# Performance work log

Hardware: AMD Instinct MI355X
Metric: run time of the kernel (lower is better)

The kernel has to match this reference:

```python
import jax, jax.numpy as jnp
import numpy as np

N = 100000
E = 3200000
D_IN = 128
D_H = 128
K = 3


def setup_inputs() -> dict:
    key = jax.random.key(0)
    ks = jax.random.split(key, 8)
    x = jax.random.normal(ks[0], (N, D_IN), dtype=jnp.float32)
    src = jax.random.randint(ks[1], (E,), 0, N, dtype=jnp.int32)
    dst = jax.random.randint(ks[2], (E,), 0, N, dtype=jnp.int32)
    s = 1.0 / np.sqrt(D_H)
    W1 = jax.random.normal(ks[3], (D_IN, D_H), dtype=jnp.float32) * s
    b1 = jnp.zeros((D_H,), jnp.float32)
    W2 = jax.random.normal(ks[4], (D_H, D_H), dtype=jnp.float32) * s
    b2 = jnp.zeros((D_H,), jnp.float32)
    Wf1 = jax.random.normal(ks[5], (D_H, D_H), dtype=jnp.float32) * s
    bf1 = jnp.zeros((D_H,), jnp.float32)
    Wf2 = jax.random.normal(ks[6], (D_H, 1), dtype=jnp.float32) * s
    bf2 = jnp.zeros((1,), jnp.float32)
    return {"x": x, "src": src, "dst": dst, "W1": W1, "b1": b1, "W2": W2,
            "b2": b2, "Wf1": Wf1, "bf1": bf1, "Wf2": Wf2, "bf2": bf2}


def _sg_propagate(h, src, dst, norm, k):
    # DGL SGConv: k hops of h <- D^{-1/2} A D^{-1/2} h (in-degree norm, clamp>=1)
    for _ in range(k):
        h = h * norm                                   # [N, d]
        h = jax.ops.segment_sum(h[src], dst, num_segments=N)  # SpMM hop
        h = h * norm
    return h


def reference(x, src, dst, W1, b1, W2, b2, Wf1, bf1, Wf2, bf2):
    deg = jax.ops.segment_sum(jnp.ones((E,), jnp.float32), dst, num_segments=N)
    norm = jnp.clip(deg, 1.0, None) ** -0.5            # [N]
    norm = norm[:, None]
    # conv_1: SGConv(k=3) -> linear -> ReLU
    h = _sg_propagate(x, src, dst, norm, K)
    h = jax.nn.relu(h @ W1 + b1)
    # conv_2
    h = _sg_propagate(h, src, dst, norm, K)
    h = jax.nn.relu(h @ W2 + b2)
    # dgl.mean_nodes over the single graph -> [1, D_H]
    hg = jnp.mean(h, axis=0, keepdims=True)
    h = jax.nn.relu(hg @ Wf1 + bf1)
    out = jax.nn.relu(h @ Wf2 + bf2)
    return jax.nn.sigmoid(out)                         # [1, 1]
```

## Files before the change

kernel.cpp:

```cpp
#include <hip/hip_runtime.h>
#include <hip/hip_fp16.h>
#include <math.h>

#define NN 100000
#define EE 3200000
#define D 128
#define NB 391
#define NBLK 256
#define ECHUNK ((EE + NBLK - 1) / NBLK)
#define NSTRIP (NN / 32)

#define SCALE_R 6.0f
#define SCALE_G 512.0f

typedef _Float16 half8 __attribute__((ext_vector_type(8)));
typedef float floatx16 __attribute__((ext_vector_type(16)));
typedef float v2f __attribute__((ext_vector_type(2)));

__global__ __launch_bounds__(256) void coarse_count(const int* __restrict__ dst,
                                                    int* __restrict__ coarse_cnt) {
    __shared__ int hist[NB];
    for (int i = threadIdx.x; i < NB; i += 256) hist[i] = 0;
    __syncthreads();
    int e0 = blockIdx.x * ECHUNK;
    int e1 = e0 + ECHUNK; if (e1 > EE) e1 = EE;
    for (int e = e0 + threadIdx.x; e < e1; e += 256)
        atomicAdd(&hist[dst[e] >> 8], 1);
    __syncthreads();
    for (int i = threadIdx.x; i < NB; i += 256)
        if (hist[i]) atomicAdd(&coarse_cnt[i], hist[i]);
}

__global__ __launch_bounds__(512) void coarse_scan(const int* __restrict__ coarse_cnt,
                                                   int* __restrict__ coarse_off,
                                                   int* __restrict__ coarse_cursor) {
    __shared__ int s[512];
    int t = threadIdx.x;
    int v = (t < NB) ? coarse_cnt[t] : 0;
    s[t] = v;
    __syncthreads();
    for (int off = 1; off < 512; off <<= 1) {
        int x = (t >= off) ? s[t - off] : 0;
        __syncthreads();
        s[t] += x;
        __syncthreads();
    }
    int excl = s[t] - v;
    if (t < NB) { coarse_off[t] = excl; coarse_cursor[t] = excl; }
    if (t == NB) coarse_off[NB] = excl;
}

__global__ __launch_bounds__(256) void coarse_scatter(const int* __restrict__ src,
                                                      const int* __restrict__ dst,
                                                      int* __restrict__ coarse_cursor,
                                                      int2* __restrict__ ebuf) {
    __shared__ int hist[NB];
    __shared__ int base[NB];
    for (int i = threadIdx.x; i < NB; i += 256) hist[i] = 0;
    __syncthreads();
    int e0 = blockIdx.x * ECHUNK;
    int e1 = e0 + ECHUNK; if (e1 > EE) e1 = EE;
    for (int e = e0 + threadIdx.x; e < e1; e += 256)
        atomicAdd(&hist[dst[e] >> 8], 1);
    __syncthreads();
    for (int i = threadIdx.x; i < NB; i += 256) {
        int c = hist[i];
        base[i] = c ? atomicAdd(&coarse_cursor[i], c) : 0;
    }
    __syncthreads();
    for (int e = e0 + threadIdx.x; e < e1; e += 256) {
        int d = dst[e];
        int pos = atomicAdd(&base[d >> 8], 1);
        ebuf[pos] = make_int2(src[e], d);
    }
}

__global__ __launch_bounds__(256) void fine_sort(const int2* __restrict__ ebuf,
                                                 const int* __restrict__ coarse_off,
                                                 int* __restrict__ rowptr,
                                                 float* __restrict__ norm,
                                                 int* __restrict__ csr) {
    __shared__ int cnt[256];
    __shared__ int sbuf[256];
    int b = blockIdx.x;
    int t = threadIdx.x;
    int e0 = coarse_off[b], e1 = coarse_off[b + 1];
    int n0 = b << 8;
    cnt[t] = 0;
    __syncthreads();
    for (int e = e0 + t; e < e1; e += 256)
        atomicAdd(&cnt[ebuf[e].y & 255], 1);
    __syncthreads();
    int myc = cnt[t];
    sbuf[t] = myc;
    __syncthreads();
    for (int off = 1; off < 256; off <<= 1) {
        int x = (t >= off) ? sbuf[t - off] : 0;
        __syncthreads();
        sbuf[t] += x;
        __syncthreads();
    }
    int excl = sbuf[t] - myc;
    int node = n0 + t;
    if (node < NN) {
        rowptr[node] = e0 + excl;
        float dd = (float)myc;
        if (dd < 1.0f) dd = 1.0f;
        norm[node] = rsqrtf(dd);
    }
    cnt[t] = e0 + excl;
    __syncthreads();
    for (int e = e0 + t; e < e1; e += 256) {
        int2 p = ebuf[e];
        int pos = atomicAdd(&cnt[p.y & 255], 1);
        csr[pos] = p.x;
    }
    if (b == 0 && t == 0) rowptr[NN] = EE;
}

__global__ void conv_w(const float* __restrict__ W, __half* __restrict__ Wt) {
    int idx = blockIdx.x * 256 + threadIdx.x;
    if (idx < D * D) {
        int n = idx >> 7, k = idx & 127;
        Wt[idx] = __float2half_rn(W[k * D + n]);
    }
}

__global__ void convert_scale_fp8(const float4* __restrict__ x4, int* __restrict__ g,
                                  const float* __restrict__ norm) {
    int idx = blockIdx.x * 256 + threadIdx.x;
    if (idx < NN * 32) {
        int row = idx >> 5;
        float n = norm[row];
        float4 v = x4[idx];
        int w = __builtin_amdgcn_cvt_pk_fp8_f32(v.x * n, v.y * n, 0, 0);
        w = __builtin_amdgcn_cvt_pk_fp8_f32(v.z * n, v.w * n, w, 1);
        g[idx] = w;
    }
}

template <int OUT16>
__global__ __launch_bounds__(256) void gather_fp8(const int* __restrict__ rowptr,
                                                  const int* __restrict__ csr,
                                                  const int4* __restrict__ hs,
                                                  const float* __restrict__ norm,
                                                  void* __restrict__ outv, float post) {
    int node = blockIdx.x * 4 + (threadIdx.x >> 6);
    int lane = threadIdx.x & 63;
    int e = lane >> 3;
    int c = lane & 7;
    int p0 = rowptr[node], p1 = rowptr[node + 1];
    float acc[16];
#pragma unroll
    for (int i = 0; i < 16; ++i) acc[i] = 0.0f;
    for (int p = p0 + e; p < p1; p += 8) {
        int s = csr[p];
        int4 v = hs[(size_t)s * 8 + c];
        v2f f;
        f = __builtin_amdgcn_cvt_pk_f32_fp8(v.x, 0); acc[0] += f.x;  acc[1] += f.y;
        f = __builtin_amdgcn_cvt_pk_f32_fp8(v.x, 1); acc[2] += f.x;  acc[3] += f.y;
        f = __builtin_amdgcn_cvt_pk_f32_fp8(v.y, 0); acc[4] += f.x;  acc[5] += f.y;
        f = __builtin_amdgcn_cvt_pk_f32_fp8(v.y, 1); acc[6] += f.x;  acc[7] += f.y;
        f = __builtin_amdgcn_cvt_pk_f32_fp8(v.z, 0); acc[8] += f.x;  acc[9] += f.y;
        f = __builtin_amdgcn_cvt_pk_f32_fp8(v.z, 1); acc[10] += f.x; acc[11] += f.y;
        f = __builtin_amdgcn_cvt_pk_f32_fp8(v.w, 0); acc[12] += f.x; acc[13] += f.y;
        f = __builtin_amdgcn_cvt_pk_f32_fp8(v.w, 1); acc[14] += f.x; acc[15] += f.y;
    }
#pragma unroll
    for (int off = 8; off < 64; off <<= 1) {
#pragma unroll
        for (int i = 0; i < 16; ++i) acc[i] += __shfl_xor(acc[i], off, 64);
    }
    if (e == 0) {
        float n = norm[node];
        float m = (OUT16 ? n : n * n) * post;
#pragma unroll
        for (int i = 0; i < 16; ++i) acc[i] *= m;
        if (OUT16) {
            union { int4 q; __half2 h[4]; } u0, u1;
#pragma unroll
            for (int i = 0; i < 4; ++i) {
                u0.h[i] = __floats2half2_rn(acc[2 * i], acc[2 * i + 1]);
                u1.h[i] = __floats2half2_rn(acc[8 + 2 * i], acc[9 + 2 * i]);
            }
            int4* o = (int4*)((__half*)outv + (size_t)node * D + c * 16);
            o[0] = u0.q;
            o[1] = u1.q;
        } else {
            int4 w;
            w.x = __builtin_amdgcn_cvt_pk_fp8_f32(acc[0], acc[1], 0, 0);
            w.x = __builtin_amdgcn_cvt_pk_fp8_f32(acc[2], acc[3], w.x, 1);
            w.y = __builtin_amdgcn_cvt_pk_fp8_f32(acc[4], acc[5], 0, 0);
            w.y = __builtin_amdgcn_cvt_pk_fp8_f32(acc[6], acc[7], w.y, 1);
            w.z = __builtin_amdgcn_cvt_pk_fp8_f32(acc[8], acc[9], 0, 0);
            w.z = __builtin_amdgcn_cvt_pk_fp8_f32(acc[10], acc[11], w.z, 1);
            w.w = __builtin_amdgcn_cvt_pk_fp8_f32(acc[12], acc[13], 0, 0);
            w.w = __builtin_amdgcn_cvt_pk_fp8_f32(acc[14], acc[15], w.w, 1);
            ((int4*)outv)[(size_t)node * 8 + c] = w;
        }
    }
}

__global__ __launch_bounds__(256) void gemm1_mfma(const __half* __restrict__ H,
                                                  const __half* __restrict__ Wt,
                                                  const float* __restrict__ b,
                                                  const float* __restrict__ norm,
                                                  char* __restrict__ out8) {
    int lane = threadIdx.x & 63;
    int w = threadIdx.x >> 6;
    int m = lane & 31;
    int q = lane >> 5;
    int col = w * 32 + m;
    half8 bf[8];
    const half8* wp = (const half8*)(Wt + (size_t)col * D + q * 8);
#pragma unroll
    for (int kc = 0; kc < 8; ++kc) bf[kc] = wp[kc * 2];
    float bc = b[col];
    for (int s = blockIdx.x; s < NSTRIP; s += gridDim.x) {
        int r0 = s * 32;
        floatx16 acc;
#pragma unroll
        for (int i = 0; i < 16; ++i) acc[i] = 0.0f;
        const half8* hp = (const half8*)(H + (size_t)(r0 + m) * D + q * 8);
#pragma unroll
        for (int kc = 0; kc < 8; ++kc)
            acc = __builtin_amdgcn_mfma_f32_32x32x16_f16(hp[kc * 2], bf[kc], acc, 0, 0, 0);
#pragma unroll
        for (int r = 0; r < 16; ++r) {
            int row = r0 + (r & 3) + 8 * (r >> 2) + 4 * q;
            float v = fmaxf(acc[r] + bc, 0.0f) * norm[row] * SCALE_G;
            int pk = __builtin_amdgcn_cvt_pk_fp8_f32(v, v, 0, 0);
            out8[(size_t)row * D + col] = (char)(pk & 0xff);
        }
    }
}

__global__ __launch_bounds__(256) void gemm2_mfma_colsum(const __half* __restrict__ H,
                                                         const __half* __restrict__ Wt,
                                                         const float* __restrict__ b,
                                                         float* __restrict__ colsum) {
    int lane = threadIdx.x & 63;
    int w = threadIdx.x >> 6;
    int m = lane & 31;
    int q = lane >> 5;
    int col = w * 32 + m;
    half8 bf[8];
    const half8* wp = (const half8*)(Wt + (size_t)col * D + q * 8);
#pragma unroll
    for (int kc = 0; kc < 8; ++kc) bf[kc] = wp[kc * 2];
    float bc = b[col];
    float csum = 0.0f;
    for (int s = blockIdx.x; s < NSTRIP; s += gridDim.x) {
        int r0 = s * 32;
        floatx16 acc;
#pragma unroll
        for (int i = 0; i < 16; ++i) acc[i] = 0.0f;
        const half8* hp = (const half8*)(H + (size_t)(r0 + m) * D + q * 8);
#pragma unroll
        for (int kc = 0; kc < 8; ++kc)
            acc = __builtin_amdgcn_mfma_f32_32x32x16_f16(hp[kc * 2], bf[kc], acc, 0, 0, 0);
#pragma unroll
        for (int r = 0; r < 16; ++r) csum += fmaxf(acc[r] + bc, 0.0f);
    }
    csum += __shfl_down(csum, 32);
    if (lane < 32) atomicAdd(&colsum[col], csum);
}

__global__ __launch_bounds__(128) void final_mlp(const float* __restrict__ colsum,
                                                 const float* __restrict__ Wf1,
                                                 const float* __restrict__ bf1,
                                                 const float* __restrict__ Wf2,
                                                 const float* __restrict__ bf2,
                                                 float* __restrict__ out) {
    __shared__ float hg[D];
    __shared__ float red[D];
    int j = threadIdx.x;
    hg[j] = colsum[j] * (1.0f / (float)NN);
    __syncthreads();
    float acc = bf1[j];
#pragma unroll 16
    for (int k = 0; k < D; ++k)
        acc = fmaf(hg[k], Wf1[k * D + j], acc);
    acc = fmaxf(acc, 0.0f);
    red[j] = acc * Wf2[j];
    __syncthreads();
    for (int s = 64; s > 0; s >>= 1) {
        if (j < s) red[j] += red[j + s];
        __syncthreads();
    }
    if (j == 0) {
        float o = red[0] + bf2[0];
        o = fmaxf(o, 0.0f);
        out[0] = 1.0f / (1.0f + expf(-o));
    }
}

extern "C" void kernel_launch(void* const* d_in, const int* in_sizes, int n_in,
                              void* d_out, int out_size, void* d_ws, size_t ws_size,
                              hipStream_t stream) {
    const float* x   = (const float*)d_in[0];
    const int*   src = (const int*)d_in[1];
    const int*   dst = (const int*)d_in[2];
    const float* W1  = (const float*)d_in[3];
    const float* b1  = (const float*)d_in[4];
    const float* W2  = (const float*)d_in[5];
    const float* b2  = (const float*)d_in[6];
    const float* Wf1 = (const float*)d_in[7];
    const float* bf1 = (const float*)d_in[8];
    const float* Wf2 = (const float*)d_in[9];
    const float* bf2 = (const float*)d_in[10];
    float* out = (float*)d_out;

    char* ws = (char*)d_ws;
    constexpr size_t OFF_CC   = 0;
    constexpr size_t OFF_CO   = 4096;
    constexpr size_t OFF_CU   = 8192;
    constexpr size_t OFF_CS   = 12288;
    constexpr size_t OFF_WT1  = 16384;
    constexpr size_t OFF_WT2  = OFF_WT1 + 32768;
    constexpr size_t OFF_RP   = OFF_WT2 + 32768;
    constexpr size_t OFF_NORM = OFF_RP + 400128;
    constexpr size_t OFF_EBUF = OFF_NORM + 400128;
    constexpr size_t OFF_CSR  = OFF_EBUF + (size_t)EE * 8;
    constexpr size_t OFF_A8   = OFF_CSR + (size_t)EE * 4;
    constexpr size_t OFF_B8   = OFF_A8 + (size_t)NN * D;
    constexpr size_t OFF_H16  = OFF_B8 + (size_t)NN * D;
    int*    ccnt   = (int*)(ws + OFF_CC);
    int*    coff   = (int*)(ws + OFF_CO);
    int*    ccur   = (int*)(ws + OFF_CU);
    float*  colsum = (float*)(ws + OFF_CS);
    __half* Wt1    = (__half*)(ws + OFF_WT1);
    __half* Wt2    = (__half*)(ws + OFF_WT2);
    int*    rowptr = (int*)(ws + OFF_RP);
    float*  norm   = (float*)(ws + OFF_NORM);
    int2*   ebuf   = (int2*)(ws + OFF_EBUF);
    int*    csr    = (int*)(ws + OFF_CSR);
    char*   bufA8  = ws + OFF_A8;
    char*   bufB8  = ws + OFF_B8;
    __half* bufH   = (__half*)(ws + OFF_H16);

    const int nT = 256;
    const int gridC = (NN * 32 + nT - 1) / nT;
    const int gridG = NN / 4;

    const float invR2  = 1.0f / (SCALE_R * SCALE_R);
    const float invGR2 = 1.0f / (SCALE_G * SCALE_R * SCALE_R);

    hipMemsetAsync(ccnt, 0, (size_t)NB * 4, stream);
    coarse_count<<<NBLK, 256, 0, stream>>>(dst, ccnt);
    coarse_scan<<<1, 512, 0, stream>>>(ccnt, coff, ccur);
    coarse_scatter<<<NBLK, 256, 0, stream>>>(src, dst, ccur, ebuf);
    fine_sort<<<NB, 256, 0, stream>>>(ebuf, coff, rowptr, norm, csr);

    conv_w<<<64, 256, 0, stream>>>(W1, Wt1);
    conv_w<<<64, 256, 0, stream>>>(W2, Wt2);

    convert_scale_fp8<<<gridC, nT, 0, stream>>>((const float4*)x, (int*)bufA8, norm);
    gather_fp8<0><<<gridG, 256, 0, stream>>>(rowptr, csr, (const int4*)bufA8, norm, bufB8, SCALE_R);
    gather_fp8<0><<<gridG, 256, 0, stream>>>(rowptr, csr, (const int4*)bufB8, norm, bufA8, SCALE_R);
    gather_fp8<1><<<gridG, 256, 0, stream>>>(rowptr, csr, (const int4*)bufA8, norm, bufH, invR2);

    gemm1_mfma<<<625, 256, 0, stream>>>(bufH, Wt1, b1, norm, bufA8);

    gather_fp8<0><<<gridG, 256, 0, stream>>>(rowptr, csr, (const int4*)bufA8, norm, bufB8, SCALE_R);
    gather_fp8<0><<<gridG, 256, 0, stream>>>(rowptr, csr, (const int4*)bufB8, norm, bufA8, SCALE_R);
    gather_fp8<1><<<gridG, 256, 0, stream>>>(rowptr, csr, (const int4*)bufA8, norm, bufH, invGR2);

    hipMemsetAsync(colsum, 0, D * 4, stream);
    gemm2_mfma_colsum<<<250, 256, 0, stream>>>(bufH, Wt2, b2, colsum);

    final_mlp<<<1, 128, 0, stream>>>(colsum, Wf1, bf1, Wf2, bf2, out);
}
```

Baseline: 713.3 us.

## Replace atomic coarse bucketing with per-block histogram scan and 1024-block scatter

Edge bucketing by destination bin now stores a histogram for each block in a bin-major matrix. A scan over each bin, then over the bin totals, gives every block its exact output offsets. The scatter no longer recomputes its histogram or claims offsets with global atomics, and it runs on 1024 blocks instead of 256 for more parallelism. The cost is one more kernel launch and a 1.6 MB histogram buffer.

```diff
diff --git a/kernel.cpp b/kernel.cpp
--- a/kernel.cpp
+++ b/kernel.cpp
@@ -6,8 +6,8 @@
 #define EE 3200000
 #define D 128
 #define NB 391
-#define NBLK 256
-#define ECHUNK ((EE + NBLK - 1) / NBLK)
+#define NBLK2 1024
+#define ECH2 (EE / NBLK2)
 #define NSTRIP (NN / 32)
 
 #define SCALE_R 6.0f
@@ -17,26 +17,46 @@
 typedef float floatx16 __attribute__((ext_vector_type(16)));
 typedef float v2f __attribute__((ext_vector_type(2)));
 
-__global__ __launch_bounds__(256) void coarse_count(const int* __restrict__ dst,
-                                                    int* __restrict__ coarse_cnt) {
+__global__ __launch_bounds__(256) void block_hist(const int* __restrict__ dst,
+                                                  int* __restrict__ bh) {
     __shared__ int hist[NB];
     for (int i = threadIdx.x; i < NB; i += 256) hist[i] = 0;
     __syncthreads();
-    int e0 = blockIdx.x * ECHUNK;
-    int e1 = e0 + ECHUNK; if (e1 > EE) e1 = EE;
-    for (int e = e0 + threadIdx.x; e < e1; e += 256)
+    int e0 = blockIdx.x * ECH2;
+    for (int e = e0 + threadIdx.x; e < e0 + ECH2; e += 256)
         atomicAdd(&hist[dst[e] >> 8], 1);
     __syncthreads();
     for (int i = threadIdx.x; i < NB; i += 256)
-        if (hist[i]) atomicAdd(&coarse_cnt[i], hist[i]);
-}
-
-__global__ __launch_bounds__(512) void coarse_scan(const int* __restrict__ coarse_cnt,
-                                                   int* __restrict__ coarse_off,
-                                                   int* __restrict__ coarse_cursor) {
+        bh[i * NBLK2 + blockIdx.x] = hist[i];
+}
+
+__global__ __launch_bounds__(256) void bin_scan(int* __restrict__ bh,
+                                                int* __restrict__ bintot) {
+    __shared__ int ts[256];
+    int i = blockIdx.x;
+    int t = threadIdx.x;
+    int4 v = ((int4*)(bh + i * NBLK2))[t];
+    int s = v.x + v.y + v.z + v.w;
+    ts[t] = s;
+    __syncthreads();
+    for (int off = 1; off < 256; off <<= 1) {
+        int x = (t >= off) ? ts[t - off] : 0;
+        __syncthreads();
+        ts[t] += x;
+        __syncthreads();
+    }
+    int run = ts[t] - s;
+    int4 o;
+    o.x = run; o.y = run + v.x; o.z = o.y + v.y; o.w = o.z + v.z;
+    ((int4*)(bh + i * NBLK2))[t] = o;
+    if (t == 255) bintot[i] = ts[255];
+}
+
+__global__ __launch_bounds__(512) void tiny_scan(const int* __restrict__ bintot,
+                                                 int* __restrict__ coff) {
     __shared__ int s[512];
     int t = threadIdx.x;
-    int v = (t < NB) ? coarse_cnt[t] : 0;
+    int v = (t < NB) ? bintot[t] : 0;
     s[t] = v;
     __syncthreads();
     for (int off = 1; off < 512; off <<= 1) {
@@ -46,29 +66,21 @@
         __syncthreads();
     }
     int excl = s[t] - v;
-    if (t < NB) { coarse_off[t] = excl; coarse_cursor[t] = excl; }
-    if (t == NB) coarse_off[NB] = excl;
-}
-
-__global__ __launch_bounds__(256) void coarse_scatter(const int* __restrict__ src,
-                                                      const int* __restrict__ dst,
-                                                      int* __restrict__ coarse_cursor,
-                                                      int2* __restrict__ ebuf) {
-    __shared__ int hist[NB];
+    if (t <= NB) coff[t] = excl;
+}
+
+__global__ __launch_bounds__(256) void scatter2(const int* __restrict__ src,
+                                                const int* __restrict__ dst,
+                                                const int* __restrict__ bh,
+                                                const int* __restrict__ coff,
+                                                int2* __restrict__ ebuf) {
     __shared__ int base[NB];
-    for (int i = threadIdx.x; i < NB; i += 256) hist[i] = 0;
-    __syncthreads();
-    int e0 = blockIdx.x * ECHUNK;
-    int e1 = e0 + ECHUNK; if (e1 > EE) e1 = EE;
-    for (int e = e0 + threadIdx.x; e < e1; e += 256)
-        atomicAdd(&hist[dst[e] >> 8], 1);
-    __syncthreads();
-    for (int i = threadIdx.x; i < NB; i += 256) {
-        int c = hist[i];
-        base[i] = c ? atomicAdd(&coarse_cursor[i], c) : 0;
-    }
-    __syncthreads();
-    for (int e = e0 + threadIdx.x; e < e1; e += 256) {
+    int b = blockIdx.x;
+    for (int i = threadIdx.x; i < NB; i += 256)
+        base[i] = coff[i] + bh[i * NBLK2 + b];
+    __syncthreads();
+    int e0 = b * ECH2;
+    for (int e = e0 + threadIdx.x; e < e0 + ECH2; e += 256) {
         int d = dst[e];
         int pos = atomicAdd(&base[d >> 8], 1);
         ebuf[pos] = make_int2(src[e], d);
@@ -312,27 +324,27 @@
     float* out = (float*)d_out;
 
     char* ws = (char*)d_ws;
-    constexpr size_t OFF_CC   = 0;
-    constexpr size_t OFF_CO   = 4096;
-    constexpr size_t OFF_CU   = 8192;
-    constexpr size_t OFF_CS   = 12288;
-    constexpr size_t OFF_WT1  = 16384;
+    constexpr size_t OFF_BT   = 0;
+    constexpr size_t OFF_CO   = 2048;
+    constexpr size_t OFF_CS   = 4096;
+    constexpr size_t OFF_WT1  = 8192;
     constexpr size_t OFF_WT2  = OFF_WT1 + 32768;
     constexpr size_t OFF_RP   = OFF_WT2 + 32768;
     constexpr size_t OFF_NORM = OFF_RP + 400128;
-    constexpr size_t OFF_EBUF = OFF_NORM + 400128;
+    constexpr size_t OFF_BH   = OFF_NORM + 400128;
+    constexpr size_t OFF_EBUF = OFF_BH + (size_t)NB * NBLK2 * 4;
     constexpr size_t OFF_CSR  = OFF_EBUF + (size_t)EE * 8;
     constexpr size_t OFF_A8   = OFF_CSR + (size_t)EE * 4;
     constexpr size_t OFF_B8   = OFF_A8 + (size_t)NN * D;
     constexpr size_t OFF_H16  = OFF_B8 + (size_t)NN * D;
-    int*    ccnt   = (int*)(ws + OFF_CC);
+    int*    bintot = (int*)(ws + OFF_BT);
     int*    coff   = (int*)(ws + OFF_CO);
-    int*    ccur   = (int*)(ws + OFF_CU);
     float*  colsum = (float*)(ws + OFF_CS);
     __half* Wt1    = (__half*)(ws + OFF_WT1);
     __half* Wt2    = (__half*)(ws + OFF_WT2);
     int*    rowptr = (int*)(ws + OFF_RP);
     float*  norm   = (float*)(ws + OFF_NORM);
+    int*    bh     = (int*)(ws + OFF_BH);
     int2*   ebuf   = (int2*)(ws + OFF_EBUF);
     int*    csr    = (int*)(ws + OFF_CSR);
     char*   bufA8  = ws + OFF_A8;
@@ -346,10 +358,10 @@
     const float invR2  = 1.0f / (SCALE_R * SCALE_R);
     const float invGR2 = 1.0f / (SCALE_G * SCALE_R * SCALE_R);
 
-    hipMemsetAsync(ccnt, 0, (size_t)NB * 4, stream);
-    coarse_count<<<NBLK, 256, 0, stream>>>(dst, ccnt);
-    coarse_scan<<<1, 512, 0, stream>>>(ccnt, coff, ccur);
-    coarse_scatter<<<NBLK, 256, 0, stream>>>(src, dst, ccur, ebuf);
+    block_hist<<<NBLK2, 256, 0, stream>>>(dst, bh);
+    bin_scan<<<NB, 256, 0, stream>>>(bh, bintot);
+    tiny_scan<<<1, 512, 0, stream>>>(bintot, coff);
+    scatter2<<<NBLK2, 256, 0, stream>>>(src, dst, bh, coff, ebuf);
     fine_sort<<<NB, 256, 0, stream>>>(ebuf, coff, rowptr, norm, csr);
 
     conv_w<<<64, 256, 0, stream>>>(W1, Wt1);
```

Result: faster. 680.4 us (-4.6%).
